# Performance work log

Measured on AMD Instinct MI355X. Metric: run time of the kernel, lower is better.

Reference implementation:

```python
import jax, jax.numpy as jnp
import numpy as np

EPS = 1e-8


def setup_inputs() -> dict:
    key = jax.random.key(0)
    k1, k2, k3 = jax.random.split(key, 3)
    B, N, M, C = 4, 4096, 16384, 256
    xyz = jax.random.normal(k1, (B * N, 3), dtype=jnp.float32)
    new_xyz = jax.random.normal(k2, (B * M, 3), dtype=jnp.float32)
    feat = jax.random.normal(k3, (B * N, C), dtype=jnp.float32)
    offset = jnp.arange(1, B + 1, dtype=jnp.int64) * N      # [4096, 8192, 12288, 16384]
    new_offset = jnp.arange(1, B + 1, dtype=jnp.int64) * M  # [16384, ..., 65536]
    return {"xyz": xyz, "new_xyz": new_xyz, "feat": feat,
            "offset": offset, "new_offset": new_offset, "k": 3}


def _interpolate(xyz_b, new_xyz_b, feat_b, k):
    # xyz_b: [B,N,3], new_xyz_b: [B,M,3], feat_b: [B,N,C]
    # pairwise squared distances via GEMM: [B,M,N]
    q2 = jnp.sum(new_xyz_b * new_xyz_b, axis=-1, keepdims=True)        # [B,M,1]
    s2 = jnp.sum(xyz_b * xyz_b, axis=-1)[:, None, :]                   # [B,1,N]
    cross = jnp.einsum('bmd,bnd->bmn', new_xyz_b, xyz_b)               # [B,M,N]
    d2 = q2 + s2 - 2.0 * cross                                         # [B,M,N]
    neg_d2, idx = jax.lax.top_k(-d2, k)                                # [B,M,k]
    dist = jnp.sqrt(jnp.maximum(-neg_d2, 1e-12))                       # euclidean, like knnquery
    dist_recip = 1.0 / (dist + EPS)
    weight = dist_recip / jnp.sum(dist_recip, axis=-1, keepdims=True)  # [B,M,k]
    gathered = jax.vmap(lambda f, i: f[i])(feat_b, idx)                # [B,M,k,C]
    return jnp.einsum('bmkc,bmk->bmc', gathered, weight)               # [B,M,C]


def reference(xyz, new_xyz, feat, offset, new_offset, k):
    B = offset.shape[0]
    N = xyz.shape[0] // B
    M = new_xyz.shape[0] // B
    C = feat.shape[1]
    # uniform offsets -> reshape into per-cloud batches
    out = _interpolate(xyz.reshape(B, N, 3), new_xyz.reshape(B, M, 3),
                       feat.reshape(B, N, C), k)
    return out.reshape(B * M, C)
```

## Files before the change

kernel.cpp:

```cpp
#include <hip/hip_runtime.h>
#include <float.h>


#define QPB   64
#define SPLIT 8
#define KEY_INIT 0x7FEFFFFFFFFFFFFFULL

__global__ void pack_pts(const float* __restrict__ xyz,
                         float4* __restrict__ pts, int total) {
    int i = blockIdx.x * blockDim.x + threadIdx.x;
    if (i < total) {
        const float sx = xyz[(size_t)i * 3 + 0];
        const float sy = xyz[(size_t)i * 3 + 1];
        const float sz = xyz[(size_t)i * 3 + 2];
        const float s2 = __fadd_rn(__fadd_rn(__fmul_rn(sx, sx), __fmul_rn(sy, sy)),
                                   __fmul_rn(sz, sz));
        pts[i] = make_float4(sx, sy, sz, s2);
    }
}

__device__ __forceinline__ double mk_key(float d2, int j) {
    unsigned long long u =
        ((unsigned long long)(unsigned)__float_as_uint(d2) << 32) | (unsigned)j;
    return __longlong_as_double(u);
}

template <int CHUNK>
__global__ __launch_bounds__(512, 8) void fp_knn_main(
    const float* __restrict__ new_xyz,
    const float4* __restrict__ pts,
    const float4* __restrict__ feat4,
    float4* __restrict__ out4,
    int N, int blocks_per_batch)
{
    __shared__ double s_k[SPLIT][QPB][3];
    __shared__ float  s_w[QPB][3];
    __shared__ int    s_j[QPB][3];

    int g = blockIdx.x;
    if (gridDim.x == 1024 && blocks_per_batch == 256) {
        const int xcd = g & 7, slot = g >> 3;
        g = (xcd >> 1) * 256 + (xcd & 1) * 128 + slot;
    }

    const int tid = threadIdx.x;
    const int q   = tid & (QPB - 1);
    const int b   = g / blocks_per_batch;
    const int src_base = b * N;
    const int m = g * QPB + q;

    const float qx = new_xyz[(size_t)m * 3 + 0];
    const float qy = new_xyz[(size_t)m * 3 + 1];
    const float qz = new_xyz[(size_t)m * 3 + 2];
    const float q2 = __fadd_rn(__fadd_rn(__fmul_rn(qx, qx), __fmul_rn(qy, qy)),
                               __fmul_rn(qz, qz));

    const int s_u   = __builtin_amdgcn_readfirstlane(tid >> 6);
    const int cbase = s_u * CHUNK;
    const float4* __restrict__ cp = pts + src_base + cbase;

    double k0 = __longlong_as_double(KEY_INIT);
    double k1 = k0, k2 = k0;

    constexpr int G  = 4;
    constexpr int NG = CHUNK / G;
    float4 buf[2][G];

    #pragma unroll
    for (int t = 0; t < G; ++t) buf[0][t] = cp[t];

    auto process = [&](const float4 p, int cj) {
        const float cross = __fadd_rn(
            __fadd_rn(__fmul_rn(qx, p.x), __fmul_rn(qy, p.y)),
            __fmul_rn(qz, p.z));
        const float d2 = __fadd_rn(q2, p.w) - (cross + cross);
        const double key = mk_key(d2, cj);
        const double n0 = fmin(key, k0);
        const double n1 = fmin(fmax(key, k0), k1);
        const double n2 = fmin(fmax(key, k1), k2);
        k0 = n0; k1 = n1; k2 = n2;
    };

    #pragma unroll 2
    for (int gi = 0; gi < NG - 1; ++gi) {
        const float4* nx = cp + (gi + 1) * G;
        #pragma unroll
        for (int t = 0; t < G; ++t) buf[(gi + 1) & 1][t] = nx[t];
        #pragma unroll
        for (int t = 0; t < G; ++t)
            process(buf[gi & 1][t], cbase + gi * G + t);
    }
    #pragma unroll
    for (int t = 0; t < G; ++t)
        process(buf[(NG - 1) & 1][t], cbase + (NG - 1) * G + t);

    s_k[s_u][q][0] = k0; s_k[s_u][q][1] = k1; s_k[s_u][q][2] = k2;
    __syncthreads();

    if (tid < QPB) {
        double m0 = __longlong_as_double(KEY_INIT), m1 = m0, m2 = m0;
        #pragma unroll
        for (int ss = 0; ss < SPLIT; ++ss) {
            #pragma unroll
            for (int r = 0; r < 3; ++r) {
                const double d = s_k[ss][tid][r];
                const double n0 = fmin(d, m0);
                const double n1 = fmin(fmax(d, m0), m1);
                const double n2 = fmin(fmax(d, m1), m2);
                m0 = n0; m1 = n1; m2 = n2;
            }
        }
        unsigned long long u0 = __double_as_longlong(m0);
        unsigned long long u1 = __double_as_longlong(m1);
        unsigned long long u2 = __double_as_longlong(m2);
        const float d0 = __uint_as_float((unsigned)(u0 >> 32));
        const float d1 = __uint_as_float((unsigned)(u1 >> 32));
        const float d2 = __uint_as_float((unsigned)(u2 >> 32));
        const float e0 = sqrtf(fmaxf(d0, 1e-12f));
        const float e1 = sqrtf(fmaxf(d1, 1e-12f));
        const float e2 = sqrtf(fmaxf(d2, 1e-12f));
        const float r0 = 1.0f / (e0 + 1e-8f);
        const float r1 = 1.0f / (e1 + 1e-8f);
        const float r2 = 1.0f / (e2 + 1e-8f);
        const float rs = r0 + r1 + r2;
        s_w[tid][0] = r0 / rs; s_w[tid][1] = r1 / rs; s_w[tid][2] = r2 / rs;
        s_j[tid][0] = (int)(u0 & 0xffffffffu);
        s_j[tid][1] = (int)(u1 & 0xffffffffu);
        s_j[tid][2] = (int)(u2 & 0xffffffffu);
    }
    __syncthreads();

    const int lane  = tid & 63;
    const int wv    = tid >> 6;
    const int qbase = g * QPB;
    #pragma unroll 2
    for (int t = 0; t < QPB / SPLIT; ++t) {
        const int qq = wv * (QPB / SPLIT) + t;
        const int   a0 = s_j[qq][0], a1 = s_j[qq][1], a2 = s_j[qq][2];
        const float u0 = s_w[qq][0], u1 = s_w[qq][1], u2 = s_w[qq][2];
        const float4 f0 = feat4[(size_t)(src_base + a0) * 64 + lane];
        const float4 f1 = feat4[(size_t)(src_base + a1) * 64 + lane];
        const float4 f2 = feat4[(size_t)(src_base + a2) * 64 + lane];
        float4 o;
        o.x = u0 * f0.x + u1 * f1.x + u2 * f2.x;
        o.y = u0 * f0.y + u1 * f1.y + u2 * f2.y;
        o.z = u0 * f0.z + u1 * f1.z + u2 * f2.z;
        o.w = u0 * f0.w + u1 * f1.w + u2 * f2.w;
        out4[(size_t)(qbase + qq) * 64 + lane] = o;
    }
}

__global__ void fp_knn_generic(
    const float* __restrict__ new_xyz, const float* __restrict__ xyz,
    const float* __restrict__ feat, float* __restrict__ out,
    int N, int M, int Btot)
{
    const int m = blockIdx.x * blockDim.x + threadIdx.x;
    if (m >= Btot * M) return;
    const int b = m / M;
    const int src_base = b * N;
    const float qx = new_xyz[(size_t)m * 3 + 0];
    const float qy = new_xyz[(size_t)m * 3 + 1];
    const float qz = new_xyz[(size_t)m * 3 + 2];
    const float q2 = __fadd_rn(__fadd_rn(__fmul_rn(qx, qx), __fmul_rn(qy, qy)),
                               __fmul_rn(qz, qz));
    double k0 = __longlong_as_double(KEY_INIT), k1 = k0, k2 = k0;
    for (int j = 0; j < N; ++j) {
        const float sx = xyz[(size_t)(src_base + j) * 3 + 0];
        const float sy = xyz[(size_t)(src_base + j) * 3 + 1];
        const float sz = xyz[(size_t)(src_base + j) * 3 + 2];
        const float s2 = __fadd_rn(__fadd_rn(__fmul_rn(sx, sx), __fmul_rn(sy, sy)),
                                   __fmul_rn(sz, sz));
        const float cross = __fadd_rn(
            __fadd_rn(__fmul_rn(qx, sx), __fmul_rn(qy, sy)), __fmul_rn(qz, sz));
        const float d2 = __fadd_rn(q2, s2) - (cross + cross);
        const double key = mk_key(d2, j);
        const double n0 = fmin(key, k0);
        const double n1 = fmin(fmax(key, k0), k1);
        const double n2 = fmin(fmax(key, k1), k2);
        k0 = n0; k1 = n1; k2 = n2;
    }
    unsigned long long u0 = __double_as_longlong(k0);
    unsigned long long u1 = __double_as_longlong(k1);
    unsigned long long u2 = __double_as_longlong(k2);
    const float e0 = sqrtf(fmaxf(__uint_as_float((unsigned)(u0 >> 32)), 1e-12f));
    const float e1 = sqrtf(fmaxf(__uint_as_float((unsigned)(u1 >> 32)), 1e-12f));
    const float e2 = sqrtf(fmaxf(__uint_as_float((unsigned)(u2 >> 32)), 1e-12f));
    const float r0 = 1.0f / (e0 + 1e-8f);
    const float r1 = 1.0f / (e1 + 1e-8f);
    const float r2 = 1.0f / (e2 + 1e-8f);
    const float rs = r0 + r1 + r2;
    const float w0 = r0 / rs, w1 = r1 / rs, w2 = r2 / rs;
    const int a0 = (int)(u0 & 0xffffffffu), a1 = (int)(u1 & 0xffffffffu),
              a2 = (int)(u2 & 0xffffffffu);
    const int C = 256;
    for (int c = 0; c < C; ++c) {
        out[(size_t)m * C + c] =
            w0 * feat[(size_t)(src_base + a0) * C + c] +
            w1 * feat[(size_t)(src_base + a1) * C + c] +
            w2 * feat[(size_t)(src_base + a2) * C + c];
    }
}

extern "C" void kernel_launch(void* const* d_in, const int* in_sizes, int n_in,
                              void* d_out, int out_size, void* d_ws, size_t ws_size,
                              hipStream_t stream) {
    const float* xyz     = (const float*)d_in[0];
    const float* new_xyz = (const float*)d_in[1];
    const float* feat    = (const float*)d_in[2];
    float* out = (float*)d_out;

    const int B = in_sizes[3];
    const int N = in_sizes[0] / (3 * B);
    const int M = in_sizes[1] / (3 * B);

    const size_t need = (size_t)(B * N) * sizeof(float4);
    const bool fast = (N % SPLIT == 0) && (N / SPLIT == 512) &&
                      (M % QPB == 0) && (ws_size >= need);
    if (fast) {
        pack_pts<<<(B * N + 255) / 256, 256, 0, stream>>>(xyz, (float4*)d_ws, B * N);
        const int blocks = (B * M) / QPB;
        fp_knn_main<512><<<blocks, 512, 0, stream>>>(
            new_xyz, (const float4*)d_ws, (const float4*)feat, (float4*)out,
            N, M / QPB);
    } else {
        fp_knn_generic<<<(B * M + 255) / 256, 256, 0, stream>>>(
            new_xyz, xyz, feat, out, N, M, B);
    }
}
```

Baseline: 213.1 us.

## Process two queries per lane with packed float2 distance math

Each thread now handles two query points (128 queries per block instead of 64), so every loaded candidate point is reused for two distance computations. The distance arithmetic uses two-wide float vectors so the compiler can emit packed FP32 instructions, with contraction turned off to keep the rounding identical. The grid halves, the XCD remap and the gather unroll are adjusted to match, and the launch-bounds occupancy hint drops from 8 to 4. In exchange each thread carries twice the top-k registers, which lowers occupancy, and the grid has fewer blocks.

Result: no change. 215.3 us (+1.0%).

```diff
diff --git a/kernel.cpp b/kernel.cpp
--- a/kernel.cpp
+++ b/kernel.cpp
@@ -2,9 +2,12 @@
 #include <float.h>
 
 
-#define QPB   64
+#define QPL   2
+#define QPB   128
 #define SPLIT 8
 #define KEY_INIT 0x7FEFFFFFFFFFFFFFULL
+
+typedef float v2f __attribute__((ext_vector_type(2)));
 
 __global__ void pack_pts(const float* __restrict__ xyz,
                          float4* __restrict__ pts, int total) {
@@ -26,7 +29,7 @@
 }
 
 template <int CHUNK>
-__global__ __launch_bounds__(512, 8) void fp_knn_main(
+__global__ __launch_bounds__(512, 4) void fp_knn_main(
     const float* __restrict__ new_xyz,
     const float4* __restrict__ pts,
     const float4* __restrict__ feat4,
@@ -38,31 +41,42 @@
     __shared__ int    s_j[QPB][3];
 
     int g = blockIdx.x;
-    if (gridDim.x == 1024 && blocks_per_batch == 256) {
+    if (gridDim.x == 512 && blocks_per_batch == 128) {
         const int xcd = g & 7, slot = g >> 3;
-        g = (xcd >> 1) * 256 + (xcd & 1) * 128 + slot;
-    }
-
-    const int tid = threadIdx.x;
-    const int q   = tid & (QPB - 1);
-    const int b   = g / blocks_per_batch;
+        g = (xcd >> 1) * 128 + (xcd & 1) * 64 + slot;
+    }
+
+    const int tid  = threadIdx.x;
+    const int lane = tid & 63;
+    const int b    = g / blocks_per_batch;
     const int src_base = b * N;
-    const int m = g * QPB + q;
-
-    const float qx = new_xyz[(size_t)m * 3 + 0];
-    const float qy = new_xyz[(size_t)m * 3 + 1];
-    const float qz = new_xyz[(size_t)m * 3 + 2];
-    const float q2 = __fadd_rn(__fadd_rn(__fmul_rn(qx, qx), __fmul_rn(qy, qy)),
-                               __fmul_rn(qz, qz));
-
-    const int s_u   = __builtin_amdgcn_readfirstlane(tid >> 6);
-    const int cbase = s_u * CHUNK;
+    const int m0 = g * QPB + lane;
+    const int m1 = m0 + 64;
+
+    const float q0x = new_xyz[(size_t)m0 * 3 + 0];
+    const float q0y = new_xyz[(size_t)m0 * 3 + 1];
+    const float q0z = new_xyz[(size_t)m0 * 3 + 2];
+    const float q1x = new_xyz[(size_t)m1 * 3 + 0];
+    const float q1y = new_xyz[(size_t)m1 * 3 + 1];
+    const float q1z = new_xyz[(size_t)m1 * 3 + 2];
+    const float q02 = __fadd_rn(__fadd_rn(__fmul_rn(q0x, q0x), __fmul_rn(q0y, q0y)),
+                                __fmul_rn(q0z, q0z));
+    const float q12 = __fadd_rn(__fadd_rn(__fmul_rn(q1x, q1x), __fmul_rn(q1y, q1y)),
+                                __fmul_rn(q1z, q1z));
+    const v2f qx2 = {q0x, q1x};
+    const v2f qy2 = {q0y, q1y};
+    const v2f qz2 = {q0z, q1z};
+    const v2f q22 = {q02, q12};
+
+    const int cw    = tid >> 6;
+    const int cbase = cw * CHUNK;
     const float4* __restrict__ cp = pts + src_base + cbase;
 
-    double k0 = __longlong_as_double(KEY_INIT);
-    double k1 = k0, k2 = k0;
-
-    constexpr int G  = 4;
+    double k00 = __longlong_as_double(KEY_INIT);
+    double k01 = k00, k02 = k00;
+    double k10 = k00, k11 = k00, k12 = k00;
+
+    constexpr int G  = 8;
     constexpr int NG = CHUNK / G;
     float4 buf[2][G];
 
@@ -70,15 +84,29 @@
     for (int t = 0; t < G; ++t) buf[0][t] = cp[t];
 
     auto process = [&](const float4 p, int cj) {
-        const float cross = __fadd_rn(
-            __fadd_rn(__fmul_rn(qx, p.x), __fmul_rn(qy, p.y)),
-            __fmul_rn(qz, p.z));
-        const float d2 = __fadd_rn(q2, p.w) - (cross + cross);
-        const double key = mk_key(d2, cj);
-        const double n0 = fmin(key, k0);
-        const double n1 = fmin(fmax(key, k0), k1);
-        const double n2 = fmin(fmax(key, k1), k2);
-        k0 = n0; k1 = n1; k2 = n2;
+        #pragma clang fp contract(off)
+        const v2f px = {p.x, p.x};
+        const v2f py = {p.y, p.y};
+        const v2f pz = {p.z, p.z};
+        const v2f pw = {p.w, p.w};
+        const v2f t0 = qx2 * px;
+        const v2f t1 = qy2 * py;
+        const v2f t2 = t0 + t1;
+        const v2f t3 = qz2 * pz;
+        const v2f cr = t2 + t3;
+        const v2f qs = q22 + pw;
+        const v2f cc = cr + cr;
+        const v2f d2 = qs - cc;
+        const double ka = mk_key(d2.x, cj);
+        const double kb = mk_key(d2.y, cj);
+        const double a0 = fmin(ka, k00);
+        const double a1 = fmin(fmax(ka, k00), k01);
+        const double a2 = fmin(fmax(ka, k01), k02);
+        k00 = a0; k01 = a1; k02 = a2;
+        const double b0 = fmin(kb, k10);
+        const double b1 = fmin(fmax(kb, k10), k11);
+        const double b2 = fmin(fmax(kb, k11), k12);
+        k10 = b0; k11 = b1; k12 = b2;
     };
 
     #pragma unroll 2
@@ -94,25 +122,26 @@
     for (int t = 0; t < G; ++t)
         process(buf[(NG - 1) & 1][t], cbase + (NG - 1) * G + t);
 
-    s_k[s_u][q][0] = k0; s_k[s_u][q][1] = k1; s_k[s_u][q][2] = k2;
+    s_k[cw][lane][0]      = k00; s_k[cw][lane][1]      = k01; s_k[cw][lane][2]      = k02;
+    s_k[cw][lane + 64][0] = k10; s_k[cw][lane + 64][1] = k11; s_k[cw][lane + 64][2] = k12;
     __syncthreads();
 
     if (tid < QPB) {
-        double m0 = __longlong_as_double(KEY_INIT), m1 = m0, m2 = m0;
+        double m0k = __longlong_as_double(KEY_INIT), m1k = m0k, m2k = m0k;
         #pragma unroll
         for (int ss = 0; ss < SPLIT; ++ss) {
             #pragma unroll
             for (int r = 0; r < 3; ++r) {
                 const double d = s_k[ss][tid][r];
-                const double n0 = fmin(d, m0);
-                const double n1 = fmin(fmax(d, m0), m1);
-                const double n2 = fmin(fmax(d, m1), m2);
-                m0 = n0; m1 = n1; m2 = n2;
+                const double n0 = fmin(d, m0k);
+                const double n1 = fmin(fmax(d, m0k), m1k);
+                const double n2 = fmin(fmax(d, m1k), m2k);
+                m0k = n0; m1k = n1; m2k = n2;
             }
         }
-        unsigned long long u0 = __double_as_longlong(m0);
-        unsigned long long u1 = __double_as_longlong(m1);
-        unsigned long long u2 = __double_as_longlong(m2);
+        unsigned long long u0 = __double_as_longlong(m0k);
+        unsigned long long u1 = __double_as_longlong(m1k);
+        unsigned long long u2 = __double_as_longlong(m2k);
         const float d0 = __uint_as_float((unsigned)(u0 >> 32));
         const float d1 = __uint_as_float((unsigned)(u1 >> 32));
         const float d2 = __uint_as_float((unsigned)(u2 >> 32));
@@ -130,10 +159,9 @@
     }
     __syncthreads();
 
-    const int lane  = tid & 63;
     const int wv    = tid >> 6;
     const int qbase = g * QPB;
-    #pragma unroll 2
+    #pragma unroll 4
     for (int t = 0; t < QPB / SPLIT; ++t) {
         const int qq = wv * (QPB / SPLIT) + t;
         const int   a0 = s_j[qq][0], a1 = s_j[qq][1], a2 = s_j[qq][2];
```
